# Optimization experiments

Measured on AMD Instinct MI355X. Metric: run time of the kernel, lower is better.

Reference implementation:

```python
import jax, jax.numpy as jnp
import numpy as np
from jax.scipy.linalg import lu as jax_lu

B, C = 4096, 1024


def setup_inputs() -> dict:
    key = jax.random.key(0)
    k0, k1, k2 = jax.random.split(key, 3)
    x0 = jax.random.normal(k0, (B, C), dtype=jnp.float32)
    x1 = jax.random.normal(k1, (B, C), dtype=jnp.float32)
    W = jax.random.normal(k2, (C, C), dtype=jnp.float32)
    return {"x0": x0, "x1": x1, "W": W}


def reference(x0, x1, W):
    # Edge 1 (in=concat, out=split): MHD_concat sorts by abs index then cats on dim=1;
    # MHD_split splits by node_channels on dim=1 and maps back to node order.
    c = jnp.concatenate([x0, x1], axis=1)            # [B, 2C]
    n3, n4 = c[:, :C], c[:, C:]                      # split -> nodes 3, 4

    # Edge 2 (in=matmul, out=svd): abs-index sorted pair (n3, W) -> torch.matmul
    m = n3 @ W                                        # [B, C]
    # MHD_svd: flatten (already 2D), full_matrices=False, components U,S,Vh -> nodes
    U, S, Vh = jnp.linalg.svd(m, full_matrices=False) # U:[B,C] S:[C] Vh:[C,C]

    # Edge 3 (out=lu): MHD_lu -> torch.linalg.lu gives P, L, U (components L,U,P order)
    P, L, Uu = jax_lu(n4)                             # P:[B,B] L:[B,C] Uu:[C,C]

    # Node tails: 'avg' = stack.mean(0), 'max' = stack.max(0) elementwise
    a = (U + L) * 0.5                                 # avg tail, [B, C]
    b = jnp.maximum(Vh, Uu)                           # max tail, [C, C]

    # Final combining node: matmul edge + S scaling + permutation routing
    out = (a @ b) * S[None, :] + P @ a                # [B, C]
    return out
```

## Files before the change

### kernel.cpp

```cpp
#include <hip/hip_runtime.h>

#define AG __HIP_MEMORY_SCOPE_AGENT

__device__ __forceinline__ void gridbar(int* bar, int nblk) {
  __threadfence();
  __syncthreads();
  if (threadIdx.x == 0) {
    int g = __hip_atomic_load(bar + 1, __ATOMIC_RELAXED, AG);
    int prev = __hip_atomic_fetch_add(bar, 1, __ATOMIC_ACQ_REL, AG);
    if (prev == nblk - 1) {
      __hip_atomic_store(bar, 0, __ATOMIC_RELAXED, AG);
      __hip_atomic_fetch_add(bar + 1, 1, __ATOMIC_ACQ_REL, AG);
    } else {
      while (__hip_atomic_load(bar + 1, __ATOMIC_ACQUIRE, AG) == g)
        __builtin_amdgcn_s_sleep(16);
    }
  }
  __syncthreads();
}

__global__ __launch_bounds__(256) void gemm64(const float* __restrict__ A, const float* __restrict__ B,
                                              float* __restrict__ C, int M, int N, int K,
                                              const float* __restrict__ Sdiv) {
  __shared__ float As[16][65], Bs[16][65];
  const int tid = threadIdx.x;
  const int n0 = blockIdx.x * 64, m0 = blockIdx.y * 64;
  const int tx = tid & 15, ty = tid >> 4;
  const int lka = tid & 15, lma = tid >> 4;
  const int lnb = tid & 63, lkb = tid >> 6;
  float acc[4][4] = {{0.f}};
  for (int k0 = 0; k0 < K; k0 += 16) {
#pragma unroll
    for (int p = 0; p < 4; ++p)
      As[lka][lma + p * 16] = A[(m0 + lma + p * 16) * K + k0 + lka];
#pragma unroll
    for (int p = 0; p < 4; ++p)
      Bs[lkb + p * 4][lnb] = B[(k0 + lkb + p * 4) * N + n0 + lnb];
    __syncthreads();
#pragma unroll
    for (int kk = 0; kk < 16; ++kk) {
      float a0 = As[kk][ty * 4 + 0], a1 = As[kk][ty * 4 + 1], a2 = As[kk][ty * 4 + 2], a3 = As[kk][ty * 4 + 3];
      float b0 = Bs[kk][tx * 4 + 0], b1 = Bs[kk][tx * 4 + 1], b2 = Bs[kk][tx * 4 + 2], b3 = Bs[kk][tx * 4 + 3];
      acc[0][0] += a0 * b0; acc[0][1] += a0 * b1; acc[0][2] += a0 * b2; acc[0][3] += a0 * b3;
      acc[1][0] += a1 * b0; acc[1][1] += a1 * b1; acc[1][2] += a1 * b2; acc[1][3] += a1 * b3;
      acc[2][0] += a2 * b0; acc[2][1] += a2 * b1; acc[2][2] += a2 * b2; acc[2][3] += a2 * b3;
      acc[3][0] += a3 * b0; acc[3][1] += a3 * b1; acc[3][2] += a3 * b2; acc[3][3] += a3 * b3;
    }
    __syncthreads();
  }
#pragma unroll
  for (int i2 = 0; i2 < 4; ++i2) {
    int row = m0 + ty * 4 + i2;
#pragma unroll
    for (int j2 = 0; j2 < 4; ++j2) {
      int col = n0 + tx * 4 + j2;
      float v = acc[i2][j2];
      if (Sdiv) v /= fmaxf(Sdiv[col], 1e-12f);
      C[row * N + col] = v;
    }
  }
}

__global__ __launch_bounds__(1024) void qr_persist(float* __restrict__ A, int* bar) {
  const int tid = threadIdx.x, bid = blockIdx.x;
  const int co = tid & 15, rc = tid >> 4;
  const int c = bid * 16 + co;
  __shared__ double part[17][64];
  __shared__ double wsh[16];
  const int M = 4096, N = 1024;
  int pendJ = -1; float pendBeta = 0.f;
  for (int j = 0; j < N; ++j) {
    if (pendJ >= 0 && bid == (pendJ >> 4) && tid == 0) A[pendJ * N + pendJ] = pendBeta;
    double acc = 0, accN = 0;
    if (c > j) {
      for (int r = j + 1 + rc; r < M; r += 64) {
        double aj = (double)A[r * N + j];
        acc += aj * (double)A[r * N + c];
        if (co == 0) accN += aj * aj;
      }
    } else if (co == 0) {
      for (int r = j + 1 + rc; r < M; r += 64) { double aj = (double)A[r * N + j]; accN += aj * aj; }
    }
    part[co][rc] = acc;
    if (co == 0) part[16][rc] = accN;
    __syncthreads();
    for (int off = 32; off > 0; off >>= 1) {
      if (rc < off) { part[co][rc] += part[co][rc + off]; if (co == 0) part[16][rc] += part[16][rc + off]; }
      __syncthreads();
    }
    double xnorm2 = part[16][0];
    double alpha = (double)A[j * N + j];
    double beta, tau, s;
    if (xnorm2 == 0.0) { beta = alpha; tau = 0.0; s = 0.0; }
    else {
      beta = -copysign(sqrt(alpha * alpha + xnorm2), alpha);
      tau = (beta - alpha) / beta;
      s = 1.0 / (alpha - beta);
    }
    if (rc == 0 && c > j) wsh[co] = (double)A[j * N + c] + s * part[co][0];
    __syncthreads();
    if (tau != 0.0 && c > j) {
      double tw = tau * wsh[co];
      for (int r = j + rc; r < M; r += 64) {
        double vr = (r == j) ? 1.0 : s * (double)A[r * N + j];
        A[r * N + c] -= (float)(vr * tw);
      }
    }
    pendJ = j; pendBeta = (float)beta;
    gridbar(bar, 64);
  }
  if (bid == ((N - 1) >> 4) && tid == 0) A[(N - 1) * N + (N - 1)] = pendBeta;
}

__global__ void copyR(const float* __restrict__ Qw, double* __restrict__ R64) {
  int idx = blockIdx.x * 256 + threadIdx.x;
  int i = idx >> 10, j = idx & 1023;
  R64[idx] = (j >= i) ? (double)Qw[i * 1024 + j] : 0.0;
}

__global__ __launch_bounds__(1024) void gebrd_persist(double* __restrict__ A, double* __restrict__ d,
                                                      double* __restrict__ e, double* __restrict__ taup,
                                                      double* __restrict__ svec, int* bar) {
  const int tid = threadIdx.x, bid = blockIdx.x;
  const int co = tid & 15, rc = tid >> 4;
  const int ro = tid >> 6, cc = tid & 63;
  const int c = bid * 16 + co;
  const int rr = bid * 16 + ro;
  __shared__ double part[17][64];
  __shared__ double wsh[16];
  const int n = 1024;
  for (int i = 0; i < n; ++i) {
    double acc = 0, accN = 0;
    if (c > i) {
      for (int r = i + 1 + rc; r < n; r += 64) {
        double ai_ = A[r * n + i];
        acc += ai_ * A[r * n + c];
        if (co == 0) accN += ai_ * ai_;
      }
    } else if (co == 0) {
      for (int r = i + 1 + rc; r < n; r += 64) { double ai_ = A[r * n + i]; accN += ai_ * ai_; }
    }
    part[co][rc] = acc;
    if (co == 0) part[16][rc] = accN;
    __syncthreads();
    for (int off = 32; off > 0; off >>= 1) {
      if (rc < off) { part[co][rc] += part[co][rc + off]; if (co == 0) part[16][rc] += part[16][rc + off]; }
      __syncthreads();
    }
    double xnorm2 = part[16][0];
    double alpha = A[i * n + i];
    double beta, tau, s;
    if (xnorm2 == 0.0) { beta = alpha; tau = 0.0; s = 0.0; }
    else { beta = -copysign(sqrt(alpha * alpha + xnorm2), alpha); tau = (beta - alpha) / beta; s = 1.0 / (alpha - beta); }
    if (rc == 0 && c > i) wsh[co] = A[i * n + c] + s * part[co][0];
    __syncthreads();
    if (tau != 0.0 && c > i) {
      double tw = tau * wsh[co];
      for (int r = i + rc; r < n; r += 64) {
        double vr = (r == i) ? 1.0 : s * A[r * n + i];
        A[r * n + c] -= vr * tw;
      }
    }
    if (bid == 0 && tid == 0) d[i] = beta;
    gridbar(bar, 64);
    if (i >= n - 1) continue;
    acc = 0; accN = 0;
    if (rr > i) {
      for (int ci = i + 2 + cc; ci < n; ci += 64) {
        double av = A[i * n + ci];
        acc += av * A[rr * n + ci];
        if (ro == 0) accN += av * av;
      }
    } else if (ro == 0) {
      for (int ci = i + 2 + cc; ci < n; ci += 64) { double av = A[i * n + ci]; accN += av * av; }
    }
    part[ro][cc] = acc;
    if (ro == 0) part[16][cc] = accN;
    __syncthreads();
    for (int off = 32; off > 0; off >>= 1) {
      if (cc < off) { part[ro][cc] += part[ro][cc + off]; if (ro == 0) part[16][cc] += part[16][cc + off]; }
      __syncthreads();
    }
    double rn2 = part[16][0];
    double ralpha = A[i * n + (i + 1)];
    double rbeta, rtau, rs;
    if (rn2 == 0.0) { rbeta = ralpha; rtau = 0.0; rs = 0.0; }
    else { rbeta = -copysign(sqrt(ralpha * ralpha + rn2), ralpha); rtau = (rbeta - ralpha) / rbeta; rs = 1.0 / (ralpha - rbeta); }
    if (cc == 0 && rr > i) wsh[ro] = A[rr * n + (i + 1)] + rs * part[ro][0];
    __syncthreads();
    if (rtau != 0.0 && rr > i) {
      double tw2 = rtau * wsh[ro];
      for (int ci = i + 1 + cc; ci < n; ci += 64) {
        double uc = (ci == i + 1) ? 1.0 : rs * A[i * n + ci];
        A[rr * n + ci] -= tw2 * uc;
      }
    }
    if (bid == 0 && tid == 0) { e[i] = rbeta; taup[i] = rtau; svec[i] = rs; }
    gridbar(bar, 64);
  }
}

struct LeafDesc { int lo[32]; int nn[32]; int sq[32]; int voff[32]; int doff[32]; };

__global__ __launch_bounds__(256) void leaves_fused(const double* __restrict__ dvec, const double* __restrict__ evec,
                                                    double* __restrict__ pool, double* __restrict__ dpool, LeafDesc ld) {
  const int li = blockIdx.x;
  const int lo = ld.lo[li], n = ld.nn[li], sq = ld.sq[li];
  double* Vout = pool + ld.voff[li];
  double* dout = dpool + ld.doff[li];
  const int M = n + sq, Mp = (M + 1) & ~1;
  __shared__ double Ta[34 * 34], Tb[34 * 34], Va[34 * 34], Vb[34 * 34];
  __shared__ double al[34], be[34];
  __shared__ int part[34], prm[34];
  int tid = threadIdx.x;
  for (int x = tid; x < Mp * Mp; x += 256) {
    int a = x / Mp, b = x - a * Mp;
    double v = 0;
    if (a < M && b < M) {
      if (a == b) {
        double dd = (a < n) ? dvec[lo + a] : 0.0;
        double ee = (a >= 1) ? evec[lo + a - 1] : 0.0;
        v = dd * dd + ee * ee;
      } else if (b == a + 1 && a < n) v = dvec[lo + a] * evec[lo + a];
      else if (a == b + 1 && b < n) v = dvec[lo + b] * evec[lo + b];
    }
    Ta[x] = v; Va[x] = (a == b) ? 1.0 : 0.0;
  }
  __syncthreads();
  double *T = Ta, *Tn = Tb, *V = Va, *Vn = Vb;
  const int nm1 = Mp - 1, half = Mp / 2;
  for (int r = 0; r < 16 * nm1; ++r) {
    int rr = r % nm1;
    for (int pp = tid; pp < half; pp += 256) {
      int p, q;
      if (pp == 0) { p = nm1; q = rr; }
      else { p = (rr + pp) % nm1; q = (rr - pp + nm1) % nm1; }
      if (p > q) { int t2 = p; p = q; q = t2; }
      double app = T[p * Mp + p], aqq = T[q * Mp + q], apq = T[p * Mp + q];
      double cč = 1.0, sč = 0.0;
      if (apq != 0.0) {
        double th = (aqq - app) / (2.0 * apq);
        double t2 = 1.0 / (fabs(th) + sqrt(1.0 + th * th));
        if (th < 0.0) t2 = -t2;
        cč = 1.0 / sqrt(1.0 + t2 * t2);
        sč = t2 * cč;
      }
      part[p] = q; part[q] = p;
      al[p] = cč; be[p] = -sč; al[q] = cč; be[q] = sč;
    }
    __syncthreads();
    for (int x = tid; x < Mp * Mp; x += 256) {
      int i = x / Mp, j = x - i * Mp;
      int pj = part[j], pi = part[i];
      double aj = al[j], bj = be[j], ai = al[i], bi = be[i];
      Tn[x] = ai * (aj * T[i * Mp + j] + bj * T[i * Mp + pj]) + bi * (aj * T[pi * Mp + j] + bj * T[pi * Mp + pj]);
      Vn[x] = aj * V[i * Mp + j] + bj * V[i * Mp + pj];
    }
    __syncthreads();
    double* t2 = T; T = Tn; Tn = t2;
    t2 = V; V = Vn; Vn = t2;
  }
  if (tid == 0) {
    for (int k = 0; k < M; ++k) prm[k] = k;
    for (int a = 0; a < M; ++a) {
      int best = a;
      for (int b = a + 1; b < M; ++b)
        if (T[prm[b] * Mp + prm[b]] < T[prm[best] * Mp + prm[best]]) best = b;
      int t3 = prm[a]; prm[a] = prm[best]; prm[best] = t3;
    }
    for (int k = 0; k < M; ++k) {
      double lam = T[prm[k] * Mp + prm[k]];
      dout[k] = sqrt(lam > 0.0 ? lam : 0.0);
    }
  }
  __syncthreads();
  for (int x = tid; x < M * M; x += 256) {
    int coord = x / M, j = x - coord * M;
    Vout[coord * M + j] = V[coord * Mp + prm[j]];
  }
}

__global__ __launch_bounds__(1024) void asmk(const double* __restrict__ Vl, int Ml, const double* __restrict__ dl,
                                             const double* __restrict__ Vr, int Mr, const double* __restrict__ dr,
                                             const double* __restrict__ dvec, const double* __restrict__ evec, int ic,
                                             double* __restrict__ dm, double* __restrict__ z, int* __restrict__ src,
                                             int* __restrict__ defl, int* __restrict__ rlist,
                                             int* __restrict__ rotp, int* __restrict__ rotq,
                                             double* __restrict__ rotc, double* __restrict__ rots,
                                             int* __restrict__ iscr, double* __restrict__ zsum2) {
  const int M = Ml + Mr;
  int t = threadIdx.x;
  __shared__ double alpha_s, beta_s;
  if (t == 0) {
    alpha_s = dvec[ic]; beta_s = evec[ic];
    dm[0] = 0.0; src[0] = 0;
    int i = 1, j = 0, k = 1;
    while (k < M) {
      bool takeleft;
      if (i < Ml && j < Mr) takeleft = (dl[i] <= dr[j]);
      else takeleft = (i < Ml);
      if (takeleft) { dm[k] = dl[i]; src[k] = i; ++i; }
      else { dm[k] = dr[j]; src[k] = Ml + j; ++j; }
      ++k;
    }
  }
  __syncthreads();
  for (int k = t; k < M; k += 1024) {
    int s = src[k];
    z[k] = (s < Ml) ? alpha_s * Vl[(Ml - 1) * Ml + s] : beta_s * Vr[s - Ml];
    defl[k] = 0;
  }
  __syncthreads();
  if (t == 0) {
    const double EPS32 = 5.9604644775390625e-8;
    double aa = fabs(alpha_s), bb = fabs(beta_s);
    double tol = aa > bb ? aa : bb;
    if (dm[M - 1] > tol) tol = dm[M - 1];
    tol = 8.0 * EPS32 * tol;
    int prev = 0, nrot = 0;
    for (int J = 1; J < M; ++J) {
      if (fabs(z[J]) <= tol) { defl[J] = 1; z[J] = 0.0; }
      else if (prev >= 0 && (dm[J] - dm[prev]) <= tol) {
        double zp = z[prev], zq = z[J];
        double tau = sqrt(zp * zp + zq * zq);
        double cč = zq / tau, sč = -zp / tau;
        z[J] = tau; z[prev] = 0.0; defl[prev] = 1;
        rotp[nrot] = prev; rotq[nrot] = J; rotc[nrot] = cč; rots[nrot] = sč; ++nrot;
        prev = J;
      } else prev = J;
    }
    int K = 0; double s2 = 0;
    for (int J = 0; J < M; ++J) if (!defl[J]) { rlist[K++] = J; s2 += z[J] * z[J]; }
    iscr[0] = K; iscr[1] = nrot; zsum2[0] = s2;
  }
}

__global__ __launch_bounds__(256) void seck(const double* __restrict__ dm, const double* __restrict__ z,
                                            const int* __restrict__ iscr, const int* __restrict__ rlist,
                                            const double* __restrict__ zsum2, double* __restrict__ troot, int M) {
  int j = blockIdx.x;
  int K = iscr[0];
  if (j >= K) return;
  __shared__ double sred[256];
  int tid = threadIdx.x;
  double dj = dm[rlist[j]];
  double lo = dj * dj, hi;
  if (j + 1 < K) { double dn = dm[rlist[j + 1]]; hi = dn * dn; }
  else { double dn = dm[rlist[K - 1]]; hi = dn * dn + zsum2[0] * 1.000001 + 1e-290; }
  double lo0 = lo, hi0 = hi;
  for (int it = 0; it < 120; ++it) {
    double mid = 0.5 * (lo + hi);
    if (!(mid > lo && mid < hi)) break;
    double p = 0;
    for (int i = tid; i < M; i += 256) {
      double zi = z[i];
      if (zi != 0.0) { double d2 = dm[i] * dm[i]; p += zi * zi / (d2 - mid); }
    }
    sred[tid] = p; __syncthreads();
    for (int off = 128; off > 0; off >>= 1) { if (tid < off) sred[tid] += sred[tid + off]; __syncthreads(); }
    double f = 1.0 + sred[0];
    __syncthreads();
    if (f < 0.0) lo = mid; else hi = mid;
  }
  if (tid == 0) {
    double tr = 0.5 * (lo + hi);
    if (tr <= lo0) tr = nextafter(lo0, hi0);
    else if (tr >= hi0) tr = nextafter(hi0, lo0);
    troot[j] = tr;
  }
}

__global__ void sortoutk(const double* __restrict__ dm, const int* __restrict__ iscr,
                         const double* __restrict__ troot, const int* __restrict__ defl,
                         int* __restrict__ omap, double* __restrict__ dnode, int M) {
  if (threadIdx.x != 0 || blockIdx.x != 0) return;
  int K = iscr[0];
  int r = 0, sidx = 0, out = 0;
  while (out < M) {
    while (sidx < M && !defl[sidx]) ++sidx;
    double dval = (sidx < M) ? dm[sidx] : 1e300;
    double rval = (r < K) ? sqrt(troot[r]) : 1e300;
    if (rval <= dval) { omap[out] = r; dnode[out] = rval; ++r; }
    else { omap[out] = (1 << 20) | sidx; dnode[out] = dval; ++sidx; }
    ++out;
  }
}

__global__ __launch_bounds__(256) void buildCk(const double* __restrict__ dm, const double* __restrict__ z,
                                               const double* __restrict__ troot, const int* __restrict__ omap,
                                               double* __restrict__ C, int M) {
  int x = blockIdx.x * 256 + threadIdx.x;
  if (x >= M * M) return;
  int i = x / M, out = x - i * M;
  int om = omap[out];
  double v;
  if (om & (1 << 20)) v = ((om & 0xFFFFF) == i) ? 1.0 : 0.0;
  else {
    double zi = z[i];
    if (zi == 0.0) v = 0.0;
    else { double d2 = dm[i] * dm[i]; v = zi / (d2 - troot[om]); }
  }
  C[i * M + out] = v;
}

__global__ __launch_bounds__(256) void rotk(double* __restrict__ C, const int* __restrict__ iscr,
                                            const int* __restrict__ rotp, const int* __restrict__ rotq,
                                            const double* __restrict__ rotc, const double* __restrict__ rots, int M) {
  int nrot = iscr[1];
  int tid = threadIdx.x;
  for (int r = nrot - 1; r >= 0; --r) {
    int p = rotp[r], q = rotq[r];
    double cč = rotc[r], sč = rots[r];
    for (int j = tid; j < M; j += 256) {
      double cp = C[p * M + j], cq = C[q * M + j];
      C[p * M + j] = cč * cp - sč * cq;
      C[q * M + j] = sč * cp + cč * cq;
    }
    __syncthreads();
  }
}

__global__ __launch_bounds__(256) void normk(double* __restrict__ C, int M) {
  int out = blockIdx.x, tid = threadIdx.x;
  __shared__ double sred[256];
  double p = 0;
  for (int i = tid; i < M; i += 256) { double v = C[i * M + out]; p += v * v; }
  sred[tid] = p; __syncthreads();
  for (int off = 128; off > 0; off >>= 1) { if (tid < off) sred[tid] += sred[tid + off]; __syncthreads(); }
  double inv = 1.0 / sqrt(sred[0]);
  __syncthreads();
  for (int i = tid; i < M; i += 256) C[i * M + out] *= inv;
}

__global__ __launch_bounds__(256) void vmergek(const double* __restrict__ Vl, int Ml,
                                               const double* __restrict__ Vr, int Mr,
                                               const double* __restrict__ C, const int* __restrict__ src,
                                               double* __restrict__ Vout, int M) {
  __shared__ double Bs[16][17], Cs[16][17];
  __shared__ int ss[16];
  int tx = threadIdx.x & 15, ty = threadIdx.x >> 4;
  int r0 = blockIdx.y * 16, o0 = blockIdx.x * 16;
  int row = r0 + ty, out = o0 + tx;
  double acc = 0;
  for (int i0 = 0; i0 < M; i0 += 16) {
    if (threadIdx.x < 16) ss[threadIdx.x] = (i0 + threadIdx.x < M) ? src[i0 + threadIdx.x] : 0;
    __syncthreads();
    int ii = i0 + ty;
    Cs[ty][tx] = (ii < M && out < M) ? C[ii * M + out] : 0.0;
    int s = ss[ty];
    int rr = r0 + tx;
    double b = 0;
    if (ii < M && rr < M) {
      if (s < Ml) { if (rr < Ml) b = Vl[rr * Ml + s]; }
      else { if (rr >= Ml) b = Vr[(rr - Ml) * Mr + (s - Ml)]; }
    }
    Bs[ty][tx] = b;
    __syncthreads();
#pragma unroll
    for (int kk = 0; kk < 16; ++kk) acc += Bs[kk][ty] * Cs[kk][tx];
    __syncthreads();
  }
  if (row < M && out < M) Vout[row * M + out] = acc;
}

__global__ void gatherVS(const double* __restrict__ Vtop, const double* __restrict__ dtop,
                         float* __restrict__ Vs, float* __restrict__ S) {
  int x = blockIdx.x * 256 + threadIdx.x;
  int coord = x >> 10, jd = x & 1023;
  Vs[coord * 1024 + jd] = (float)Vtop[coord * 1024 + (1023 - jd)];
  if (x < 1024) S[x] = (float)dtop[1023 - x];
}

__global__ __launch_bounds__(1024) void p1_nobar(float* __restrict__ VB, const double* __restrict__ A,
                                                 const double* __restrict__ taup, const double* __restrict__ svec) {
  const int tid = threadIdx.x, bid = blockIdx.x;
  const int jo = tid & 15, cc = tid >> 4;
  const int j = bid * 16 + jo;
  __shared__ double part[16][64];
  __shared__ double wsh[16];
  const int n = 1024;
  for (int i = n - 3; i >= 0; --i) {
    double rtau = taup[i];
    if (rtau == 0.0) continue;
    double rs = svec[i];
    double acc = 0;
    for (int c2 = i + 2 + cc; c2 < n; c2 += 64) acc += A[i * n + c2] * (double)VB[c2 * n + j];
    part[jo][cc] = acc;
    __syncthreads();
    for (int off = 32; off > 0; off >>= 1) { if (cc < off) part[jo][cc] += part[jo][cc + off]; __syncthreads(); }
    if (cc == 0) wsh[jo] = (double)VB[(i + 1) * n + j] + rs * part[jo][0];
    __syncthreads();
    double tw = rtau * wsh[jo];
    for (int r = i + 1 + cc; r < n; r += 64) {
      double ur = (r == i + 1) ? 1.0 : rs * A[i * n + r];
      VB[r * n + j] -= (float)(tw * ur);
    }
    __syncthreads();
  }
}

__global__ __launch_bounds__(1024) void lu_persist(float* __restrict__ A, int* __restrict__ perm, int* bar) {
  const int tid = threadIdx.x, bid = blockIdx.x;
  const int co = tid & 15, rc = tid >> 4;
  const int c0 = bid * 16;
  __shared__ float sv[1024]; __shared__ int si[1024];
  const int M = 4096, N = 1024;
  for (int i2 = bid * 1024 + tid; i2 < M; i2 += 65536) perm[i2] = i2;
  int pendK = -1, pendPiv = -1; float pendRp = 0.f;
  gridbar(bar, 64);
  for (int k = 0; k < N; ++k) {
    if (pendK >= 0 && bid == (pendK >> 4)) {
      if (tid == 0 && pendPiv != pendK) {
        float t = A[pendK * N + pendK];
        A[pendK * N + pendK] = A[pendPiv * N + pendK];
        A[pendPiv * N + pendK] = t;
      }
      __syncthreads();
      for (int r = pendK + 1 + tid; r < M; r += 1024) A[r * N + pendK] *= pendRp;
    }
    float bv = -1.f; int bi2 = 0x7fffffff;
    for (int r = k + tid; r < M; r += 1024) {
      float v = fabsf(A[r * N + k]);
      if (v > bv) { bv = v; bi2 = r; }
    }
    sv[tid] = bv; si[tid] = bi2;
    __syncthreads();
    for (int off = 512; off > 0; off >>= 1) {
      if (tid < off) {
        float v2 = sv[tid + off]; int j2 = si[tid + off];
        if (v2 > sv[tid] || (v2 == sv[tid] && j2 < si[tid])) { sv[tid] = v2; si[tid] = j2; }
      }
      __syncthreads();
    }
    int piv = si[0];
    float rp = 1.0f / A[piv * N + k];
    if (piv != k && tid < 16) {
      int c2 = c0 + tid;
      if (c2 != k) { float t = A[k * N + c2]; A[k * N + c2] = A[piv * N + c2]; A[piv * N + c2] = t; }
    }
    if (bid == 0 && tid == 0 && piv != k) { int t2 = perm[k]; perm[k] = perm[piv]; perm[piv] = t2; }
    __syncthreads();
    {
      int c2 = c0 + co;
      if (c2 > k) {
        float u = A[k * N + c2];
        float Akk = A[k * N + k];
        for (int r = k + 1 + rc; r < M; r += 64) {
          float araw = A[r * N + k];
          float vr = ((r == piv) ? Akk : araw) * rp;
          A[r * N + c2] -= vr * u;
        }
      }
    }
    pendK = k; pendPiv = piv; pendRp = rp;
    gridbar(bar, 64);
  }
  if (bid == ((N - 1) >> 4)) {
    if (tid == 0 && pendPiv != pendK) {
      float t = A[pendK * N + pendK];
      A[pendK * N + pendK] = A[pendPiv * N + pendK];
      A[pendPiv * N + pendK] = t;
    }
    __syncthreads();
    for (int r = pendK + 1 + tid; r < M; r += 1024) A[r * N + pendK] *= pendRp;
  }
}

__global__ void rowsrck(const int* __restrict__ perm, int* __restrict__ rowsrc) {
  int g = blockIdx.x * 256 + threadIdx.x;
  if (g < 4096) rowsrc[perm[g]] = g;
}

__global__ void buildB(const float* __restrict__ Vs, const float* __restrict__ LUf, float* __restrict__ B) {
  int idx = blockIdx.x * 256 + threadIdx.x;
  int i = idx >> 10, j = idx & 1023;
  float uu = (i <= j) ? LUf[i * 1024 + j] : 0.0f;
  float vh = Vs[j * 1024 + i];
  B[idx] = fmaxf(vh, uu);
}

__global__ void buildA(const float* __restrict__ U, const float* __restrict__ LUf, float* __restrict__ A) {
  int idx = blockIdx.x * 256 + threadIdx.x;
  int i = idx >> 10, j = idx & 1023;
  float l = (i > j) ? LUf[i * 1024 + j] : (i == j ? 1.0f : 0.0f);
  A[idx] = 0.5f * (U[idx] + l);
}

__global__ void epilog(float* __restrict__ out, const float* __restrict__ Amat,
                       const float* __restrict__ S, const int* __restrict__ rowsrc) {
  int idx = blockIdx.x * 256 + threadIdx.x;
  int i = idx >> 10, j = idx & 1023;
  out[idx] = out[idx] * S[j] + Amat[rowsrc[i] * 1024 + j];
}

extern "C" void kernel_launch(void* const* d_in, const int* in_sizes, int n_in,
                              void* d_out, int out_size, void* d_ws, size_t ws_size,
                              hipStream_t stream) {
  const float* x0 = (const float*)d_in[0];
  const float* x1 = (const float*)d_in[1];
  const float* W  = (const float*)d_in[2];
  float* out = (float*)d_out;
  char* ws = (char*)d_ws;

  float*  m     = (float*) (ws + 0);
  double* R64   = (double*)(ws + (16ull << 20));
  double* poolA = (double*)(ws + (24ull << 20));
  double* poolB = (double*)(ws + (33ull << 20));
  double* Cbuf  = (double*)(ws + (38ull << 20));
  char*   sm    = ws + (47ull << 20);
  float*  U     = (float*) (ws + (48ull << 20));
  float*  Qw    = U;
  float*  Am    = (float*) (ws + (64ull << 20));
  float*  Bm    = (float*) (ws + (80ull << 20));
  float*  Vs    = (float*) (ws + (84ull << 20));
  float*  LUf   = (float*) (ws + (88ull << 20));

  float*  S      = (float*) (sm + 0);
  int*    perm   = (int*)   (sm + (8   << 10));
  int*    rowsrc = (int*)   (sm + (24  << 10));
  int*    bar0   = (int*)   (sm + (56  << 10));
  double* dvec   = (double*)(sm + (60  << 10));
  double* evec   = (double*)(sm + (68  << 10));
  double* taup   = (double*)(sm + (76  << 10));
  double* svec   = (double*)(sm + (84  << 10));
  double* dpoolA = (double*)(sm + (96  << 10));
  double* dpoolB = (double*)(sm + (112 << 10));
  double* dmS    = (double*)(sm + (128 << 10));
  double* zS     = (double*)(sm + (136 << 10));
  double* trootS = (double*)(sm + (144 << 10));
  double* rotcS  = (double*)(sm + (152 << 10));
  double* rotsS  = (double*)(sm + (160 << 10));
  double* zsum2S = (double*)(sm + (168 << 10));
  int*    iscrS  = (int*)   (sm + (168 << 10) + 128);
  int*    srcS   = (int*)   (sm + (172 << 10));
  int*    deflS  = (int*)   (sm + (176 << 10));
  int*    rlistS = (int*)   (sm + (180 << 10));
  int*    omapS  = (int*)   (sm + (184 << 10));
  int*    rotpS  = (int*)   (sm + (188 << 10));
  int*    rotqS  = (int*)   (sm + (192 << 10));
  if (ws_size < (105ull << 20)) return;

  hipMemsetAsync(bar0, 0, 1024, stream);
  dim3 b256(256);

  gemm64<<<dim3(16, 64), b256, 0, stream>>>(x0, W, m, 4096, 1024, 1024, nullptr);

  hipMemcpyAsync(Qw, m, 4096ull * 1024ull * 4ull, hipMemcpyDeviceToDevice, stream);
  qr_persist<<<64, 1024, 0, stream>>>(Qw, bar0);
  copyR<<<4096, 256, 0, stream>>>(Qw, R64);
  gebrd_persist<<<64, 1024, 0, stream>>>(R64, dvec, evec, taup, svec, bar0);

  int t_lo[63], t_n[63], t_sq[63];
  t_lo[0] = 0; t_n[0] = 1024; t_sq[0] = 0;
  for (int i = 0; i < 31; ++i) {
    int lo = t_lo[i], n = t_n[i], sq = t_sq[i], nl = n / 2, nr = n - nl - 1;
    t_lo[2 * i + 1] = lo;          t_n[2 * i + 1] = nl; t_sq[2 * i + 1] = 1;
    t_lo[2 * i + 2] = lo + nl + 1; t_n[2 * i + 2] = nr; t_sq[2 * i + 2] = sq;
  }
  int Voff[63], Doff[63];
  for (int lev = 0; lev <= 5; ++lev) {
    int beg = (1 << lev) - 1, end = (1 << (lev + 1)) - 1, vo = 0, doo = 0;
    for (int i = beg; i < end; ++i) {
      Voff[i] = vo; Doff[i] = doo;
      int Mi = t_n[i] + t_sq[i];
      vo += Mi * Mi; doo += Mi;
    }
  }
  LeafDesc ld;
  for (int i = 0; i < 32; ++i) {
    int nd = 31 + i;
    ld.lo[i] = t_lo[nd]; ld.nn[i] = t_n[nd]; ld.sq[i] = t_sq[nd];
    ld.voff[i] = Voff[nd]; ld.doff[i] = Doff[nd];
  }
  leaves_fused<<<32, 256, 0, stream>>>(dvec, evec, poolB, dpoolB, ld);
  for (int lev = 4; lev >= 0; --lev) {
    double* po  = (lev & 1) ? poolB : poolA;
    double* pdo = (lev & 1) ? dpoolB : dpoolA;
    double* pc  = (lev & 1) ? poolA : poolB;
    double* pdc = (lev & 1) ? dpoolA : dpoolB;
    int beg = (1 << lev) - 1, end = (1 << (lev + 1)) - 1;
    for (int i = beg; i < end; ++i) {
      int l = 2 * i + 1, r = 2 * i + 2;
      int Ml = t_n[l] + t_sq[l], Mr = t_n[r] + t_sq[r], M = Ml + Mr;
      double *Vl = pc + Voff[l], *Vr = pc + Voff[r];
      double *dl = pdc + Doff[l], *dr = pdc + Doff[r];
      double *Vo = po + Voff[i], *dn = pdo + Doff[i];
      int ic = t_lo[i] + t_n[i] / 2;
      asmk<<<1, 1024, 0, stream>>>(Vl, Ml, dl, Vr, Mr, dr, dvec, evec, ic,
                                   dmS, zS, srcS, deflS, rlistS, rotpS, rotqS, rotcS, rotsS, iscrS, zsum2S);
      seck<<<M, 256, 0, stream>>>(dmS, zS, iscrS, rlistS, zsum2S, trootS, M);
      sortoutk<<<1, 1, 0, stream>>>(dmS, iscrS, trootS, deflS, omapS, dn, M);
      buildCk<<<(M * M + 255) / 256, 256, 0, stream>>>(dmS, zS, trootS, omapS, Cbuf, M);
      rotk<<<1, 256, 0, stream>>>(Cbuf, iscrS, rotpS, rotqS, rotcS, rotsS, M);
      normk<<<M, 256, 0, stream>>>(Cbuf, M);
      vmergek<<<dim3((M + 15) / 16, (M + 15) / 16), b256, 0, stream>>>(Vl, Ml, Vr, Mr, Cbuf, srcS, Vo, M);
    }
  }
  gatherVS<<<4096, 256, 0, stream>>>(poolA + Voff[0], dpoolA + Doff[0], Vs, S);
  p1_nobar<<<64, 1024, 0, stream>>>(Vs, R64, taup, svec);

  gemm64<<<dim3(16, 64), b256, 0, stream>>>(m, Vs, U, 4096, 1024, 1024, S);

  hipMemcpyAsync(LUf, x1, 4096ull * 1024ull * 4ull, hipMemcpyDeviceToDevice, stream);
  lu_persist<<<64, 1024, 0, stream>>>(LUf, perm, bar0);
  rowsrck<<<16, 256, 0, stream>>>(perm, rowsrc);

  buildB<<<4096, 256, 0, stream>>>(Vs, LUf, Bm);
  buildA<<<16384, 256, 0, stream>>>(U, LUf, Am);
  gemm64<<<dim3(16, 64), b256, 0, stream>>>(Am, Bm, out, 4096, 1024, 1024, nullptr);
  epilog<<<16384, 256, 0, stream>>>(out, Am, S, rowsrc);
}
```

Baseline: 251.8 ms.

## Transpose QR and LU panels to column-major with 256-block persistent kernels

The Householder QR and the LU factorization now run on transposed (column-major) copies of their inputs, so each column is contiguous and rows are read with coalesced loads instead of strided 4 KB-stride accesses. The persistent kernels grow from 64 to 256 blocks, each handling four columns with 256 threads per column, and the QR keeps the pivot and target columns in registers between the dot-product and update phases. Transpose kernels replace the device-to-device copies, and a transpose back is added after LU. The cost is the extra transpose passes and a grid barrier across 256 blocks, which needs all blocks co-resident to avoid deadlock.

After: 314.9 ms. +25.1%, slower.

```diff
diff --git a/kernel.cpp b/kernel.cpp
--- a/kernel.cpp
+++ b/kernel.cpp
@@ -17,6 +17,15 @@
     }
   }
   __syncthreads();
+}
+
+__global__ __launch_bounds__(256) void tposek(const float* __restrict__ in, float* __restrict__ out, int R, int C) {
+  __shared__ float tile[32][33];
+  int cb = blockIdx.x * 32, rb = blockIdx.y * 32;
+  int tx = threadIdx.x & 31, ty = threadIdx.x >> 5;
+  for (int yy = ty; yy < 32; yy += 8) tile[yy][tx] = in[(size_t)(rb + yy) * C + cb + tx];
+  __syncthreads();
+  for (int yy = ty; yy < 32; yy += 8) out[(size_t)(cb + yy) * R + rb + tx] = tile[tx][yy];
 }
 
 __global__ __launch_bounds__(256) void gemm64(const float* __restrict__ A, const float* __restrict__ B,
@@ -32,10 +41,10 @@
   for (int k0 = 0; k0 < K; k0 += 16) {
 #pragma unroll
     for (int p = 0; p < 4; ++p)
-      As[lka][lma + p * 16] = A[(m0 + lma + p * 16) * K + k0 + lka];
+      As[lka][lma + p * 16] = A[(size_t)(m0 + lma + p * 16) * K + k0 + lka];
 #pragma unroll
     for (int p = 0; p < 4; ++p)
-      Bs[lkb + p * 4][lnb] = B[(k0 + lkb + p * 4) * N + n0 + lnb];
+      Bs[lkb + p * 4][lnb] = B[(size_t)(k0 + lkb + p * 4) * N + n0 + lnb];
     __syncthreads();
 #pragma unroll
     for (int kk = 0; kk < 16; ++kk) {
@@ -56,40 +65,55 @@
       int col = n0 + tx * 4 + j2;
       float v = acc[i2][j2];
       if (Sdiv) v /= fmaxf(Sdiv[col], 1e-12f);
-      C[row * N + col] = v;
-    }
-  }
-}
-
-__global__ __launch_bounds__(1024) void qr_persist(float* __restrict__ A, int* bar) {
+      C[(size_t)row * N + col] = v;
+    }
+  }
+}
+
+__global__ __launch_bounds__(1024, 1) void qrT_persist(float* __restrict__ AT, int* bar) {
   const int tid = threadIdx.x, bid = blockIdx.x;
-  const int co = tid & 15, rc = tid >> 4;
-  const int c = bid * 16 + co;
-  __shared__ double part[17][64];
-  __shared__ double wsh[16];
+  const int co = tid >> 8, rl = tid & 255;
+  const int c = co * 256 + bid;
+  __shared__ double pdot[4][257];
+  __shared__ double pnorm[257];
+  __shared__ double wsh[4];
   const int M = 4096, N = 1024;
   int pendJ = -1; float pendBeta = 0.f;
   for (int j = 0; j < N; ++j) {
-    if (pendJ >= 0 && bid == (pendJ >> 4) && tid == 0) A[pendJ * N + pendJ] = pendBeta;
-    double acc = 0, accN = 0;
-    if (c > j) {
-      for (int r = j + 1 + rc; r < M; r += 64) {
-        double aj = (double)A[r * N + j];
-        acc += aj * (double)A[r * N + c];
-        if (co == 0) accN += aj * aj;
-      }
-    } else if (co == 0) {
-      for (int r = j + 1 + rc; r < M; r += 64) { double aj = (double)A[r * N + j]; accN += aj * aj; }
-    }
-    part[co][rc] = acc;
-    if (co == 0) part[16][rc] = accN;
-    __syncthreads();
-    for (int off = 32; off > 0; off >>= 1) {
-      if (rc < off) { part[co][rc] += part[co][rc + off]; if (co == 0) part[16][rc] += part[16][rc + off]; }
+    if (pendJ >= 0 && c == pendJ && rl == 0) AT[(size_t)pendJ * M + pendJ] = pendBeta;
+    const float* rowj = AT + (size_t)j * M;
+    float* rowc = AT + (size_t)c * M;
+    const bool active = (c > j);
+    float vj[16], va[16];
+    double dacc = 0.0, nacc = 0.0;
+#pragma unroll
+    for (int it = 0; it < 16; ++it) {
+      int r = j + rl + it * 256;
+      float xj = (r < M) ? rowj[r] : 0.f;
+      vj[it] = xj;
+      if (co == 0 && r > j) nacc += (double)xj * (double)xj;
+    }
+    if (active) {
+#pragma unroll
+      for (int it = 0; it < 16; ++it) {
+        int r = j + rl + it * 256;
+        float xc = (r < M) ? rowc[r] : 0.f;
+        va[it] = xc;
+        if (r > j) dacc += (double)vj[it] * (double)xc;
+      }
+    }
+    pdot[co][rl] = dacc;
+    if (co == 0) pnorm[rl] = nacc;
+    __syncthreads();
+    for (int off = 128; off > 0; off >>= 1) {
+      if (rl < off) {
+        pdot[co][rl] += pdot[co][rl + off];
+        if (co == 0) pnorm[rl] += pnorm[rl + off];
+      }
       __syncthreads();
     }
-    double xnorm2 = part[16][0];
-    double alpha = (double)A[j * N + j];
+    double xnorm2 = pnorm[0];
+    double alpha = (double)AT[(size_t)j * M + j];
     double beta, tau, s;
     if (xnorm2 == 0.0) { beta = alpha; tau = 0.0; s = 0.0; }
     else {
@@ -97,25 +121,35 @@
       tau = (beta - alpha) / beta;
       s = 1.0 / (alpha - beta);
     }
-    if (rc == 0 && c > j) wsh[co] = (double)A[j * N + c] + s * part[co][0];
-    __syncthreads();
-    if (tau != 0.0 && c > j) {
+    if (active && rl == 0) wsh[co] = (double)rowc[j] + s * pdot[co][0];
+    __syncthreads();
+    if (active && tau != 0.0) {
       double tw = tau * wsh[co];
-      for (int r = j + rc; r < M; r += 64) {
-        double vr = (r == j) ? 1.0 : s * (double)A[r * N + j];
-        A[r * N + c] -= (float)(vr * tw);
+#pragma unroll
+      for (int it = 0; it < 16; ++it) {
+        int r = j + rl + it * 256;
+        if (r < M) {
+          double vr = (r == j) ? 1.0 : s * (double)vj[it];
+          rowc[r] = va[it] - (float)(vr * tw);
+        }
       }
     }
     pendJ = j; pendBeta = (float)beta;
-    gridbar(bar, 64);
-  }
-  if (bid == ((N - 1) >> 4) && tid == 0) A[(N - 1) * N + (N - 1)] = pendBeta;
-}
-
-__global__ void copyR(const float* __restrict__ Qw, double* __restrict__ R64) {
-  int idx = blockIdx.x * 256 + threadIdx.x;
-  int i = idx >> 10, j = idx & 1023;
-  R64[idx] = (j >= i) ? (double)Qw[i * 1024 + j] : 0.0;
+    gridbar(bar, 256);
+  }
+  if (c == N - 1 && rl == 0) AT[(size_t)(N - 1) * M + (N - 1)] = pendBeta;
+}
+
+__global__ __launch_bounds__(256) void copyRT(const float* __restrict__ QT, double* __restrict__ R64) {
+  __shared__ float tile[32][33];
+  int ib = blockIdx.x * 32, jb = blockIdx.y * 32;
+  int tx = threadIdx.x & 31, ty = threadIdx.x >> 5;
+  for (int yy = ty; yy < 32; yy += 8) tile[yy][tx] = QT[(size_t)(jb + yy) * 4096 + ib + tx];
+  __syncthreads();
+  for (int yy = ty; yy < 32; yy += 8) {
+    int i = ib + yy, j = jb + tx;
+    R64[(size_t)i * 1024 + j] = (j >= i) ? (double)tile[tx][yy] : 0.0;
+  }
 }
 
 __global__ __launch_bounds__(1024) void gebrd_persist(double* __restrict__ A, double* __restrict__ d,
@@ -237,16 +271,16 @@
       else { p = (rr + pp) % nm1; q = (rr - pp + nm1) % nm1; }
       if (p > q) { int t2 = p; p = q; q = t2; }
       double app = T[p * Mp + p], aqq = T[q * Mp + q], apq = T[p * Mp + q];
-      double cč = 1.0, sč = 0.0;
+      double cj = 1.0, sj = 0.0;
       if (apq != 0.0) {
         double th = (aqq - app) / (2.0 * apq);
         double t2 = 1.0 / (fabs(th) + sqrt(1.0 + th * th));
         if (th < 0.0) t2 = -t2;
-        cč = 1.0 / sqrt(1.0 + t2 * t2);
-        sč = t2 * cč;
+        cj = 1.0 / sqrt(1.0 + t2 * t2);
+        sj = t2 * cj;
       }
       part[p] = q; part[q] = p;
-      al[p] = cč; be[p] = -sč; al[q] = cč; be[q] = sč;
+      al[p] = cj; be[p] = -sj; al[q] = cj; be[q] = sj;
     }
     __syncthreads();
     for (int x = tid; x < Mp * Mp; x += 256) {
@@ -323,9 +357,9 @@
       else if (prev >= 0 && (dm[J] - dm[prev]) <= tol) {
         double zp = z[prev], zq = z[J];
         double tau = sqrt(zp * zp + zq * zq);
-        double cč = zq / tau, sč = -zp / tau;
+        double cg = zq / tau, sg = -zp / tau;
         z[J] = tau; z[prev] = 0.0; defl[prev] = 1;
-        rotp[nrot] = prev; rotq[nrot] = J; rotc[nrot] = cč; rots[nrot] = sč; ++nrot;
+        rotp[nrot] = prev; rotq[nrot] = J; rotc[nrot] = cg; rots[nrot] = sg; ++nrot;
         prev = J;
       } else prev = J;
     }
@@ -410,11 +444,11 @@
   int tid = threadIdx.x;
   for (int r = nrot - 1; r >= 0; --r) {
     int p = rotp[r], q = rotq[r];
-    double cč = rotc[r], sč = rots[r];
+    double cg = rotc[r], sg = rots[r];
     for (int j = tid; j < M; j += 256) {
       double cp = C[p * M + j], cq = C[q * M + j];
-      C[p * M + j] = cč * cp - sč * cq;
-      C[q * M + j] = sč * cp + cč * cq;
+      C[p * M + j] = cg * cp - sg * cq;
+      C[q * M + j] = sg * cp + cg * cq;
     }
     __syncthreads();
   }
@@ -499,28 +533,31 @@
   }
 }
 
-__global__ __launch_bounds__(1024) void lu_persist(float* __restrict__ A, int* __restrict__ perm, int* bar) {
+__global__ __launch_bounds__(1024, 1) void luT_persist(float* __restrict__ AT, int* __restrict__ perm, int* bar) {
   const int tid = threadIdx.x, bid = blockIdx.x;
-  const int co = tid & 15, rc = tid >> 4;
-  const int c0 = bid * 16;
+  const int co = tid >> 8, rl = tid & 255;
+  const int c = co * 256 + bid;
   __shared__ float sv[1024]; __shared__ int si[1024];
   const int M = 4096, N = 1024;
-  for (int i2 = bid * 1024 + tid; i2 < M; i2 += 65536) perm[i2] = i2;
+  int gid = bid * 1024 + tid;
+  if (gid < M) perm[gid] = gid;
   int pendK = -1, pendPiv = -1; float pendRp = 0.f;
-  gridbar(bar, 64);
+  gridbar(bar, 256);
   for (int k = 0; k < N; ++k) {
-    if (pendK >= 0 && bid == (pendK >> 4)) {
-      if (tid == 0 && pendPiv != pendK) {
-        float t = A[pendK * N + pendK];
-        A[pendK * N + pendK] = A[pendPiv * N + pendK];
-        A[pendPiv * N + pendK] = t;
-      }
-      __syncthreads();
-      for (int r = pendK + 1 + tid; r < M; r += 1024) A[r * N + pendK] *= pendRp;
-    }
+    bool fixer = (pendK >= 0 && c == pendK);
+    if (fixer && rl == 0 && pendPiv != pendK) {
+      float t = AT[(size_t)pendK * M + pendK];
+      AT[(size_t)pendK * M + pendK] = AT[(size_t)pendK * M + pendPiv];
+      AT[(size_t)pendK * M + pendPiv] = t;
+    }
+    __syncthreads();
+    if (fixer) {
+      for (int r = pendK + 1 + rl; r < M; r += 256) AT[(size_t)pendK * M + r] *= pendRp;
+    }
+    const float* rowk = AT + (size_t)k * M;
     float bv = -1.f; int bi2 = 0x7fffffff;
     for (int r = k + tid; r < M; r += 1024) {
-      float v = fabsf(A[r * N + k]);
+      float v = fabsf(rowk[r]);
       if (v > bv) { bv = v; bi2 = r; }
     }
     sv[tid] = bv; si[tid] = bi2;
@@ -533,36 +570,35 @@
       __syncthreads();
     }
     int piv = si[0];
-    float rp = 1.0f / A[piv * N + k];
-    if (piv != k && tid < 16) {
-      int c2 = c0 + tid;
-      if (c2 != k) { float t = A[k * N + c2]; A[k * N + c2] = A[piv * N + c2]; A[piv * N + c2] = t; }
+    float rp = 1.0f / rowk[piv];
+    float Akk = rowk[k];
+    if (piv != k && rl == 0 && c != k) {
+      float t = AT[(size_t)c * M + k];
+      AT[(size_t)c * M + k] = AT[(size_t)c * M + piv];
+      AT[(size_t)c * M + piv] = t;
     }
     if (bid == 0 && tid == 0 && piv != k) { int t2 = perm[k]; perm[k] = perm[piv]; perm[piv] = t2; }
     __syncthreads();
-    {
-      int c2 = c0 + co;
-      if (c2 > k) {
-        float u = A[k * N + c2];
-        float Akk = A[k * N + k];
-        for (int r = k + 1 + rc; r < M; r += 64) {
-          float araw = A[r * N + k];
-          float vr = ((r == piv) ? Akk : araw) * rp;
-          A[r * N + c2] -= vr * u;
-        }
+    if (c > k) {
+      float* rowc = AT + (size_t)c * M;
+      float u = rowc[k];
+      for (int r = k + 1 + rl; r < M; r += 256) {
+        float araw = rowk[r];
+        float vr = ((r == piv) ? Akk : araw) * rp;
+        rowc[r] -= vr * u;
       }
     }
     pendK = k; pendPiv = piv; pendRp = rp;
-    gridbar(bar, 64);
-  }
-  if (bid == ((N - 1) >> 4)) {
-    if (tid == 0 && pendPiv != pendK) {
-      float t = A[pendK * N + pendK];
-      A[pendK * N + pendK] = A[pendPiv * N + pendK];
-      A[pendPiv * N + pendK] = t;
-    }
-    __syncthreads();
-    for (int r = pendK + 1 + tid; r < M; r += 1024) A[r * N + pendK] *= pendRp;
+    gridbar(bar, 256);
+  }
+  if (c == N - 1) {
+    if (rl == 0 && pendPiv != pendK) {
+      float t = AT[(size_t)pendK * M + pendK];
+      AT[(size_t)pendK * M + pendK] = AT[(size_t)pendK * M + pendPiv];
+      AT[(size_t)pendK * M + pendPiv] = t;
+    }
+    __syncthreads();
+    for (int r = pendK + 1 + rl; r < M; r += 256) AT[(size_t)pendK * M + r] *= pendRp;
   }
 }
 
@@ -609,8 +645,9 @@
   double* Cbuf  = (double*)(ws + (38ull << 20));
   char*   sm    = ws + (47ull << 20);
   float*  U     = (float*) (ws + (48ull << 20));
-  float*  Qw    = U;
+  float*  QT    = U;
   float*  Am    = (float*) (ws + (64ull << 20));
+  float*  LUT   = Am;
   float*  Bm    = (float*) (ws + (80ull << 20));
   float*  Vs    = (float*) (ws + (84ull << 20));
   float*  LUf   = (float*) (ws + (88ull << 20));
@@ -645,9 +682,9 @@
 
   gemm64<<<dim3(16, 64), b256, 0, stream>>>(x0, W, m, 4096, 1024, 1024, nullptr);
 
-  hipMemcpyAsync(Qw, m, 4096ull * 1024ull * 4ull, hipMemcpyDeviceToDevice, stream);
-  qr_persist<<<64, 1024, 0, stream>>>(Qw, bar0);
-  copyR<<<4096, 256, 0, stream>>>(Qw, R64);
+  tposek<<<dim3(32, 128), b256, 0, stream>>>(m, QT, 4096, 1024);
+  qrT_persist<<<256, 1024, 0, stream>>>(QT, bar0);
+  copyRT<<<dim3(32, 32), b256, 0, stream>>>(QT, R64);
   gebrd_persist<<<64, 1024, 0, stream>>>(R64, dvec, evec, taup, svec, bar0);
 
   int t_lo[63], t_n[63], t_sq[63];
@@ -701,8 +738,9 @@
 
   gemm64<<<dim3(16, 64), b256, 0, stream>>>(m, Vs, U, 4096, 1024, 1024, S);
 
-  hipMemcpyAsync(LUf, x1, 4096ull * 1024ull * 4ull, hipMemcpyDeviceToDevice, stream);
-  lu_persist<<<64, 1024, 0, stream>>>(LUf, perm, bar0);
+  tposek<<<dim3(32, 128), b256, 0, stream>>>(x1, LUT, 4096, 1024);
+  luT_persist<<<256, 1024, 0, stream>>>(LUT, perm, bar0);
+  tposek<<<dim3(128, 32), b256, 0, stream>>>(LUT, LUf, 1024, 4096);
   rowsrck<<<16, 256, 0, stream>>>(perm, rowsrc);
 
   buildB<<<4096, 256, 0, stream>>>(Vs, LUf, Bm);
```
